# Kernel optimization log

Measured on AMD Instinct MI355X. Metric: run time of the kernel, lower is better.

## Reference

```python
import jax, jax.numpy as jnp
import numpy as np

# static graph structure: B graphs, each with NPER nodes and DEG*NPER edges
B = 128        # graphs in batch
NPER = 400     # nodes per graph (fMRI atlas ROIs)
DEG = 16       # avg degree
EPG = NPER * DEG
E = B * EPG    # 819200 edges total
F_IN = 400     # num_features
H = 128        # hidden dim of GraphConv
C = 2          # num_classes
K1, K2, K3 = 320, 256, 205  # ceil(0.8*400), ceil(0.8*320), ceil(0.8*256)


def setup_inputs() -> dict:
    key = jax.random.key(0)
    ks = jax.random.split(key, 24)
    x = jax.random.normal(ks[0], (B * NPER, F_IN), dtype=jnp.float32)
    # edges constrained within each graph (PyG batched disjoint-union convention)
    src_l = jax.random.randint(ks[1], (B, EPG), 0, NPER)
    dst_l = jax.random.randint(ks[2], (B, EPG), 0, NPER)
    off = (jnp.arange(B, dtype=jnp.int32) * NPER)[:, None]
    edge_src = (src_l + off).reshape(-1).astype(jnp.int32)
    edge_dst = (dst_l + off).reshape(-1).astype(jnp.int32)
    batch = jnp.repeat(jnp.arange(B, dtype=jnp.int32), NPER)
    s = 0.05
    p = {
        'Wrel1': jax.random.normal(ks[3], (H, F_IN)) * s,
        'Wroot1': jax.random.normal(ks[4], (H, F_IN)) * s,
        'b1': jnp.zeros((H,), jnp.float32),
        'pw1': jax.random.normal(ks[5], (H,)) * s,
        'Wrel2': jax.random.normal(ks[6], (H, H)) * s,
        'Wroot2': jax.random.normal(ks[7], (H, H)) * s,
        'b2': jnp.zeros((H,), jnp.float32),
        'pw2': jax.random.normal(ks[8], (H,)) * s,
        'Wrel3': jax.random.normal(ks[9], (H, H)) * s,
        'Wroot3': jax.random.normal(ks[10], (H, H)) * s,
        'b3': jnp.zeros((H,), jnp.float32),
        'pw3': jax.random.normal(ks[11], (H,)) * s,
        'W1': jax.random.normal(ks[12], (128, 256)) * s,
        'bl1': jnp.zeros((128,), jnp.float32),
        'W2': jax.random.normal(ks[13], (64, 128)) * s,
        'bl2': jnp.zeros((64,), jnp.float32),
        'W3': jax.random.normal(ks[14], (C, 64)) * s,
        'bl3': jnp.zeros((C,), jnp.float32),
    }
    return dict(x=x, edge_src=edge_src, edge_dst=edge_dst, batch=batch, **p)


def _graph_conv(x, src, dst, emask, Wrel, b, Wroot):
    # PyG GraphConv: lin_rel(sum_j x_j) + lin_root(x_i); masked edges contribute 0
    msg = x[src] * emask[:, None]
    agg = jax.ops.segment_sum(msg, dst, num_segments=x.shape[0])
    return agg @ Wrel.T + b + x @ Wroot.T


def _topk_pool(x, src, dst, emask, w, npg, k):
    # score = x.w / ||w||; keep top-k per graph; gate kept x by tanh(score)
    score = (x @ w) / (jnp.linalg.norm(w) + 1e-16)
    vals, idx = jax.lax.top_k(score.reshape(B, npg), k)      # [B,k]
    perm = (jnp.arange(B, dtype=jnp.int32)[:, None] * npg + idx).reshape(-1)
    xk = x[perm] * jnp.tanh(vals).reshape(-1)[:, None]
    new_id = jnp.full((B * npg,), -1, jnp.int32).at[perm].set(
        jnp.arange(B * k, dtype=jnp.int32))
    ns, nd = new_id[src], new_id[dst]
    keep = (ns >= 0) & (nd >= 0)
    em2 = emask * keep.astype(emask.dtype)
    return xk, jnp.where(keep, ns, 0), jnp.where(keep, nd, 0), em2


def _readout(x, k):
    xr = x.reshape(B, k, H)
    return jnp.concatenate([xr.max(axis=1), xr.mean(axis=1)], axis=1)  # [B,256]


def reference(x, edge_src, edge_dst, batch,
              Wrel1, Wroot1, b1, pw1, Wrel2, Wroot2, b2, pw2,
              Wrel3, Wroot3, b3, pw3, W1, bl1, W2, bl2, W3, bl3):
    em = jnp.ones((E,), jnp.float32)
    h = jax.nn.relu(_graph_conv(x, edge_src, edge_dst, em, Wrel1, b1, Wroot1))
    h, s, d, em = _topk_pool(h, edge_src, edge_dst, em, pw1, NPER, K1)
    x1 = _readout(h, K1)
    h = jax.nn.relu(_graph_conv(h, s, d, em, Wrel2, b2, Wroot2))
    h, s, d, em = _topk_pool(h, s, d, em, pw2, K1, K2)
    x2 = _readout(h, K2)
    h = jax.nn.relu(_graph_conv(h, s, d, em, Wrel3, b3, Wroot3))
    h, s, d, em = _topk_pool(h, s, d, em, pw3, K2, K3)
    x3 = _readout(h, K3)
    z = x1 + x2 + x3
    z = jax.nn.relu(z @ W1.T + bl1)  # dropout is identity in eval mode
    z = jax.nn.relu(z @ W2.T + bl2)
    return jax.nn.log_softmax(z @ W3.T + bl3, axis=-1)
```

## Files before the change

kernel.cpp:

```cpp
#include <hip/hip_runtime.h>
#include <math.h>

#define BATCH 128
#define NPER 400
#define EPG 6400
#define NEDGE 819200
#define F_IN 400
#define HD 128
#define K1 320
#define K2 256
#define K3 205

typedef __bf16 bf16x8 __attribute__((ext_vector_type(8)));
typedef float f32x4 __attribute__((ext_vector_type(4)));

__device__ __forceinline__ unsigned short f2bf(float f) {
    unsigned u = __builtin_bit_cast(unsigned, f);
    unsigned r = u + 0x7fffu + ((u >> 16) & 1u);
    return (unsigned short)(r >> 16);
}
__device__ __forceinline__ float bf2f(unsigned short s) {
    unsigned u = ((unsigned)s) << 16;
    return __builtin_bit_cast(float, u);
}

__device__ __forceinline__ void async_ld16(const void* g, void* lds) {
    __builtin_amdgcn_global_load_lds(
        (const __attribute__((address_space(1))) unsigned int*)g,
        (__attribute__((address_space(3))) unsigned int*)lds, 16, 0, 0);
}

static constexpr size_t SZ_TREL = 51200ull * 128 * 4;
static constexpr size_t OFF_TREL = 0;
static constexpr size_t OFF_H    = OFF_TREL + SZ_TREL;
static constexpr size_t OFF_HP   = OFF_H + SZ_TREL;
static constexpr size_t OFF_SC   = OFF_HP + 40960ull * 128 * 4;
static constexpr size_t OFF_ES   = OFF_SC + 51200ull * 4;
static constexpr size_t OFF_ED   = OFF_ES + (size_t)NEDGE * 4;
static constexpr size_t OFF_EM   = OFF_ED + (size_t)NEDGE * 4;
static constexpr size_t OFF_Z    = OFF_EM + (size_t)NEDGE * 4;
static constexpr size_t OFF_COFF = OFF_Z + 128ull * 256 * 4;
static constexpr size_t OFF_CDEG = OFF_COFF + 51200ull * 4;
static constexpr size_t OFF_CSRC = OFF_CDEG + 51200ull * 4;
static constexpr size_t OFF_W1H  = OFF_CSRC + (size_t)NEDGE * 4;
static constexpr size_t OFF_W1L  = OFF_W1H + 16ull * 13 * 512 * 2;
static constexpr size_t OFF_W2H  = OFF_W1L + 16ull * 13 * 512 * 2;
static constexpr size_t OFF_W2L  = OFF_W2H + 16ull * 4 * 512 * 2;
static constexpr size_t OFF_W3H  = OFF_W2L + 16ull * 4 * 512 * 2;
static constexpr size_t OFF_W3L  = OFF_W3H + 16ull * 4 * 512 * 2;

__global__ __launch_bounds__(64) void prep_w_all(
    const float* __restrict__ Wrel1, const float* __restrict__ Wroot1,
    const float* __restrict__ Wrel2, const float* __restrict__ Wroot2,
    const float* __restrict__ Wrel3, const float* __restrict__ Wroot3,
    unsigned short* __restrict__ b1h, unsigned short* __restrict__ b1l,
    unsigned short* __restrict__ b2h, unsigned short* __restrict__ b2l,
    unsigned short* __restrict__ b3h, unsigned short* __restrict__ b3l) {
    const int layer = blockIdx.z;
    const int s = blockIdx.x;
    const int ntile = blockIdx.y;
    const int Ks = (layer == 0) ? 13 : 4;
    const int Kd = (layer == 0) ? F_IN : HD;
    if (s >= Ks) return;
    const float* Wrel  = (layer == 0) ? Wrel1  : (layer == 1) ? Wrel2  : Wrel3;
    const float* Wroot = (layer == 0) ? Wroot1 : (layer == 1) ? Wroot2 : Wroot3;
    unsigned short* bh = (layer == 0) ? b1h : (layer == 1) ? b2h : b3h;
    unsigned short* bl = (layer == 0) ? b1l : (layer == 1) ? b2l : b3l;
    const int t = threadIdx.x;
    const int rowin = t & 15, qd = t >> 4;
    const int n = ntile * 16 + rowin;
    const int k = s * 32 + qd * 8;
    const float* src = (n < 128) ? &Wrel[(n & 127) * Kd] : &Wroot[(n & 127) * Kd];
    unsigned short hv[8], lv[8];
#pragma unroll
    for (int e = 0; e < 8; e++) {
        float f = (k + e < Kd) ? src[k + e] : 0.f;
        unsigned short hi = f2bf(f);
        hv[e] = hi;
        lv[e] = f2bf(f - bf2f(hi));
    }
    size_t o = ((size_t)ntile * Ks + s) * 512 + (size_t)t * 8;
#pragma unroll
    for (int e = 0; e < 8; e++) { bh[o + e] = hv[e]; bl[o + e] = lv[e]; }
}

template <int Ks, int Kd>
__global__ __launch_bounds__(256) void gemm_mfma(
    const float* __restrict__ A,
    const unsigned short* __restrict__ bh_p, const unsigned short* __restrict__ bl_p,
    float* __restrict__ t_rel, float* __restrict__ h) {
    __shared__ float Alds[2][2048];
    const int tid = threadIdx.x;
    const int lane = tid & 63;
    const int wv = tid >> 6;
    const int lm = lane & 15;
    const int qd = (lane >> 4) & 3;
    const int m0 = blockIdx.x * 64;
    const int nt0 = wv * 4;

    const int srow = wv * 8 + (lane >> 3);
    const int sgr  = (lane & 7) ^ (lane >> 3);
    const size_t amax = (size_t)gridDim.x * 64 * Kd * 4 - 16;
    const char* Abyte = (const char*)A;

    const int ga = (((2 * qd)     ^ (lm & 7)) << 4);
    const int gb = (((2 * qd + 1) ^ (lm & 7)) << 4);

    f32x4 acc[4][4];
#pragma unroll
    for (int i = 0; i < 4; i++)
#pragma unroll
        for (int j = 0; j < 4; j++) acc[i][j] = (f32x4){0.f, 0.f, 0.f, 0.f};

    auto stage = [&](int buf, int s) {
#pragma unroll
        for (int p = 0; p < 2; ++p) {
            const int row = srow + p * 32;
            size_t go = (size_t)(m0 + row) * Kd * 4 + (size_t)s * 128
                        + ((size_t)sgr << 4);
            if (go > amax) go = amax;
            async_ld16(Abyte + go, &Alds[buf][p * 1024 + wv * 256]);
        }
    };

    stage(0, 0);
    __syncthreads();

#pragma unroll
    for (int s = 0; s < Ks; ++s) {
        if (s + 1 < Ks) stage((s + 1) & 1, s + 1);

        const char* Ab = (const char*)&Alds[s & 1][0];
        bf16x8 ah[4], al[4];
#pragma unroll
        for (int i = 0; i < 4; i++) {
            float4 f0, f1;
            if (s * 32 + qd * 8 < Kd) {
                const char* base = Ab + (lm + i * 16) * 128;
                f0 = *(const float4*)(base + ga);
                f1 = *(const float4*)(base + gb);
            } else {
                f0 = make_float4(0.f, 0.f, 0.f, 0.f);
                f1 = f0;
            }
            float fe[8] = {f0.x, f0.y, f0.z, f0.w, f1.x, f1.y, f1.z, f1.w};
#pragma unroll
            for (int e = 0; e < 8; e++) {
                __bf16 hb = (__bf16)fe[e];
                ah[i][e] = hb;
                al[i][e] = (__bf16)(fe[e] - (float)hb);
            }
        }
        bf16x8 bh[4], bl[4];
#pragma unroll
        for (int j = 0; j < 4; j++)
            bh[j] = *(const bf16x8*)&bh_p[((size_t)(nt0 + j) * Ks + s) * 512 + lane * 8];
#pragma unroll
        for (int j = 0; j < 4; j++)
            bl[j] = *(const bf16x8*)&bl_p[((size_t)(nt0 + j) * Ks + s) * 512 + lane * 8];
#pragma unroll
        for (int j = 0; j < 4; j++)
#pragma unroll
            for (int i = 0; i < 4; i++)
                acc[i][j] = __builtin_amdgcn_mfma_f32_16x16x32_bf16(
                    ah[i], bh[j], acc[i][j], 0, 0, 0);
#pragma unroll
        for (int j = 0; j < 4; j++)
#pragma unroll
            for (int i = 0; i < 4; i++)
                acc[i][j] = __builtin_amdgcn_mfma_f32_16x16x32_bf16(
                    al[i], bh[j], acc[i][j], 0, 0, 0);
#pragma unroll
        for (int j = 0; j < 4; j++)
#pragma unroll
            for (int i = 0; i < 4; i++)
                acc[i][j] = __builtin_amdgcn_mfma_f32_16x16x32_bf16(
                    ah[i], bl[j], acc[i][j], 0, 0, 0);

        __syncthreads();
    }
    float* out = (wv < 2) ? t_rel : h;
    const int colbase = (wv & 1) * 64;
#pragma unroll
    for (int i = 0; i < 4; i++)
#pragma unroll
        for (int j = 0; j < 4; j++) {
            int row = m0 + i * 16 + qd * 4;
            int col = colbase + j * 16 + lm;
#pragma unroll
            for (int r = 0; r < 4; r++)
                out[(size_t)(row + r) * 128 + col] = acc[i][j][r];
        }
}

__global__ __launch_bounds__(1024) void csr_build0(
    const int* __restrict__ gsrc, const int* __restrict__ gdst,
    int* __restrict__ csr_off, int* __restrict__ csr_deg, int* __restrict__ csr_src) {
    __shared__ int cnt[NPER];
    __shared__ int cur[NPER];
    __shared__ int sscan[512];
    const int g = blockIdx.x;
    const int t = threadIdx.x;
    for (int i = t; i < NPER; i += 1024) cnt[i] = 0;
    __syncthreads();
    for (int e = t; e < EPG; e += 1024) {
        int dl = gdst[g * EPG + e] - g * NPER;
        atomicAdd(&cnt[dl], 1);
    }
    __syncthreads();
    if (t < 512) sscan[t] = (t < NPER) ? cnt[t] : 0;
    __syncthreads();
    for (int d = 1; d < 512; d <<= 1) {
        int v = 0;
        if (t < 512 && t >= d) v = sscan[t - d];
        __syncthreads();
        if (t < 512 && t >= d) sscan[t] += v;
        __syncthreads();
    }
    if (t < NPER) {
        int excl = (t == 0) ? 0 : sscan[t - 1];
        int st = g * EPG + excl;
        csr_off[g * NPER + t] = st;
        csr_deg[g * NPER + t] = cnt[t];
        cur[t] = st;
    }
    __syncthreads();
    for (int e = t; e < EPG; e += 1024) {
        int eg = g * EPG + e;
        int dl = gdst[eg] - g * NPER;
        int slot = atomicAdd(&cur[dl], 1);
        csr_src[slot] = gsrc[eg];
    }
}

__global__ __launch_bounds__(256) void agg_score(
    const float* __restrict__ t_rel,
    const int* __restrict__ csr_off, const int* __restrict__ csr_deg,
    const int* __restrict__ csr_src,
    const float* __restrict__ bias, const float* __restrict__ pw,
    float* __restrict__ h, float* __restrict__ sc, int npg) {
    const int xcd = blockIdx.x & 7;
    const int j = blockIdx.x >> 3;
    const int bpg = npg >> 2;
    const int graph = xcd * (BATCH / 8) + j / bpg;
    const int nblk = j - (j / bpg) * bpg;
    const int wid = graph * npg + nblk * 4 + (threadIdx.x >> 6);
    const int lane = threadIdx.x & 63;

    const int start = csr_off[wid];
    const int deg = csr_deg[wid];
    const size_t fo = (size_t)lane * 2;
    float a0 = 0.f, a1 = 0.f, b0 = 0.f, b1 = 0.f;
    float c0 = 0.f, c1 = 0.f, d0 = 0.f, d1 = 0.f;
    int e = 0;
    for (; e + 4 <= deg; e += 4) {
        int s0 = csr_src[start + e];
        int s1 = csr_src[start + e + 1];
        int s2 = csr_src[start + e + 2];
        int s3 = csr_src[start + e + 3];
        float2 v0 = *(const float2*)&t_rel[(size_t)s0 * 128 + fo];
        float2 v1 = *(const float2*)&t_rel[(size_t)s1 * 128 + fo];
        float2 v2 = *(const float2*)&t_rel[(size_t)s2 * 128 + fo];
        float2 v3 = *(const float2*)&t_rel[(size_t)s3 * 128 + fo];
        a0 += v0.x; a1 += v0.y;
        b0 += v1.x; b1 += v1.y;
        c0 += v2.x; c1 += v2.y;
        d0 += v3.x; d1 += v3.y;
    }
    for (; e < deg; e++) {
        int s0 = csr_src[start + e];
        float2 v0 = *(const float2*)&t_rel[(size_t)s0 * 128 + fo];
        a0 += v0.x; a1 += v0.y;
    }
    a0 += b0 + c0 + d0;
    a1 += b1 + c1 + d1;

    float2 bb = *(const float2*)&bias[fo];
    size_t o = (size_t)wid * 128 + fo;
    float2 hv = *(const float2*)&h[o];
    hv.x = fmaxf(hv.x + a0 + bb.x, 0.f);
    hv.y = fmaxf(hv.y + a1 + bb.y, 0.f);
    *(float2*)&h[o] = hv;
    float2 pp = *(const float2*)&pw[fo];
    float d = hv.x * pp.x + hv.y * pp.y;
    float nr = pp.x * pp.x + pp.y * pp.y;
#pragma unroll
    for (int off = 32; off; off >>= 1) {
        d += __shfl_down(d, off, 64);
        nr += __shfl_down(nr, off, 64);
    }
    if (lane == 0) sc[wid] = d / (sqrtf(nr) + 1e-16f);
}

__device__ __forceinline__ bool rank_before(float as, int ai, float bs, int bi) {
    return (as > bs) || (as == bs && ai < bi);
}
__global__ __launch_bounds__(1024) void topk_pool(
    const float* __restrict__ sc, const float* __restrict__ h,
    float* __restrict__ hp, float* __restrict__ z,
    const int* __restrict__ gsrc, const int* __restrict__ gdst,
    int* __restrict__ es, int* __restrict__ ed, int* __restrict__ em,
    int* __restrict__ csr_off, int* __restrict__ csr_deg, int* __restrict__ csr_src,
    int npg, int k, int mode) {
    __shared__ float sk[512];
    __shared__ int si[512];
    __shared__ int nid[NPER];
    __shared__ float tgs[K1];
    __shared__ int packed[EPG];
    __shared__ int cnt[K1];
    __shared__ int cur[K1];
    __shared__ int sscan[512];
    __shared__ float pmx[8][128], psm[8][128];
    const int g = blockIdx.x;
    const int t = threadIdx.x;

    if (t < 512) {
        sk[t] = (t < npg) ? sc[g * npg + t] : -INFINITY;
        si[t] = t;
    }
    __syncthreads();
    for (int size = 2; size <= 512; size <<= 1) {
        for (int stride = size >> 1; stride; stride >>= 1) {
            if (t < 512) {
                int i = t, j = i ^ stride;
                if (j > i) {
                    bool up = ((i & size) == 0);
                    float a = sk[i], b = sk[j];
                    int ai = si[i], bi = si[j];
                    bool doswap = up ? rank_before(b, bi, a, ai)
                                     : rank_before(a, ai, b, bi);
                    if (doswap) { sk[i] = b; sk[j] = a; si[i] = bi; si[j] = ai; }
                }
            }
            __syncthreads();
        }
    }
    if (t < 512) {
        int orig = si[t];
        if (orig < npg) nid[orig] = (t < k) ? t : -1;
        if (t < k) tgs[t] = tanhf(sk[t]);
    }
    if (t < K1) cnt[t] = 0;
    __syncthreads();

    {
        const int f = t & 127;
        const int jq = t >> 7;
        float mx = -INFINITY, sm = 0.f;
        for (int j = jq; j < k; j += 8) {
            float v = h[(size_t)(g * npg + si[j]) * 128 + f] * tgs[j];
            if (mode != 2) hp[(size_t)(g * k + j) * 128 + f] = v;
            mx = fmaxf(mx, v);
            sm += v;
        }
        pmx[jq][f] = mx; psm[jq][f] = sm;
        __syncthreads();
        if (t < 128) {
            mx = pmx[0][t]; sm = psm[0][t];
#pragma unroll
            for (int q = 1; q < 8; q++) {
                mx = fmaxf(mx, pmx[q][t]);
                sm += psm[q][t];
            }
            z[g * 256 + t] += mx;
            z[g * 256 + 128 + t] += sm / (float)k;
        }
    }
    if (mode == 2) return;

    for (int e = t; e < EPG; e += 1024) {
        int eg = g * EPG + e;
        int sl, dl, m;
        if (mode == 0) { sl = gsrc[eg] - g * NPER; dl = gdst[eg] - g * NPER; m = 1; }
        else           { sl = es[eg]; dl = ed[eg]; m = em[eg]; }
        int ns = nid[sl], nd = nid[dl];
        int keep = (m && ns >= 0 && nd >= 0) ? 1 : 0;
        es[eg] = keep ? ns : 0;
        ed[eg] = keep ? nd : 0;
        em[eg] = keep;
        packed[e] = keep ? (ns | (nd << 16)) : -1;
        if (keep) atomicAdd(&cnt[nd], 1);
    }
    __syncthreads();
    if (t < 512) sscan[t] = (t < k) ? cnt[t] : 0;
    __syncthreads();
    for (int d = 1; d < 512; d <<= 1) {
        int v = 0;
        if (t < 512 && t >= d) v = sscan[t - d];
        __syncthreads();
        if (t < 512 && t >= d) sscan[t] += v;
        __syncthreads();
    }
    if (t < k) {
        int excl = (t == 0) ? 0 : sscan[t - 1];
        int st = g * EPG + excl;
        csr_off[g * k + t] = st;
        csr_deg[g * k + t] = cnt[t];
        cur[t] = st;
    }
    __syncthreads();
    for (int e = t; e < EPG; e += 1024) {
        int p = packed[e];
        if (p >= 0) {
            int ns = p & 0xffff, nd = p >> 16;
            int slot = atomicAdd(&cur[nd], 1);
            csr_src[slot] = g * k + ns;
        }
    }
}

__global__ __launch_bounds__(256) void mlp_head(const float* __restrict__ z,
                                                const float* __restrict__ W1,
                                                const float* __restrict__ bl1,
                                                const float* __restrict__ W2,
                                                const float* __restrict__ bl2,
                                                const float* __restrict__ W3,
                                                const float* __restrict__ bl3,
                                                float* __restrict__ out) {
    __shared__ float zs[256], l1[128], l2[64];
    const int g = blockIdx.x, t = threadIdx.x;
    zs[t] = z[g * 256 + t];
    __syncthreads();
    if (t < 128) {
        float s = bl1[t];
        const float* w = &W1[t * 256];
        for (int i = 0; i < 256; i++) s += w[i] * zs[i];
        l1[t] = fmaxf(s, 0.f);
    }
    __syncthreads();
    if (t < 64) {
        float s = bl2[t];
        const float* w = &W2[t * 128];
        for (int i = 0; i < 128; i++) s += w[i] * l1[i];
        l2[t] = fmaxf(s, 0.f);
    }
    __syncthreads();
    if (t == 0) {
        float a = bl3[0], b = bl3[1];
        for (int i = 0; i < 64; i++) { a += W3[i] * l2[i]; b += W3[64 + i] * l2[i]; }
        float m = fmaxf(a, b);
        float lse = m + logf(expf(a - m) + expf(b - m));
        out[g * 2 + 0] = a - lse;
        out[g * 2 + 1] = b - lse;
    }
}

extern "C" void kernel_launch(void* const* d_in, const int* in_sizes, int n_in,
                              void* d_out, int out_size, void* d_ws, size_t ws_size,
                              hipStream_t stream) {
    const float* x        = (const float*)d_in[0];
    const int*   edge_src = (const int*)d_in[1];
    const int*   edge_dst = (const int*)d_in[2];
    const float* Wrel1 = (const float*)d_in[4];
    const float* Wroot1= (const float*)d_in[5];
    const float* b1    = (const float*)d_in[6];
    const float* pw1   = (const float*)d_in[7];
    const float* Wrel2 = (const float*)d_in[8];
    const float* Wroot2= (const float*)d_in[9];
    const float* b2    = (const float*)d_in[10];
    const float* pw2   = (const float*)d_in[11];
    const float* Wrel3 = (const float*)d_in[12];
    const float* Wroot3= (const float*)d_in[13];
    const float* b3    = (const float*)d_in[14];
    const float* pw3   = (const float*)d_in[15];
    const float* W1    = (const float*)d_in[16];
    const float* bl1   = (const float*)d_in[17];
    const float* W2    = (const float*)d_in[18];
    const float* bl2   = (const float*)d_in[19];
    const float* W3    = (const float*)d_in[20];
    const float* bl3   = (const float*)d_in[21];

    char* ws = (char*)d_ws;
    float* t_rel = (float*)(ws + OFF_TREL);
    float* h     = (float*)(ws + OFF_H);
    float* hp    = (float*)(ws + OFF_HP);
    float* sc    = (float*)(ws + OFF_SC);
    int*   es    = (int*)(ws + OFF_ES);
    int*   ed    = (int*)(ws + OFF_ED);
    int*   em    = (int*)(ws + OFF_EM);
    float* z     = (float*)(ws + OFF_Z);
    int*   coff  = (int*)(ws + OFF_COFF);
    int*   cdeg  = (int*)(ws + OFF_CDEG);
    int*   csrc  = (int*)(ws + OFF_CSRC);
    unsigned short* w1h = (unsigned short*)(ws + OFF_W1H);
    unsigned short* w1l = (unsigned short*)(ws + OFF_W1L);
    unsigned short* w2h = (unsigned short*)(ws + OFF_W2H);
    unsigned short* w2l = (unsigned short*)(ws + OFF_W2L);
    unsigned short* w3h = (unsigned short*)(ws + OFF_W3H);
    unsigned short* w3l = (unsigned short*)(ws + OFF_W3L);

    hipMemsetAsync(z, 0, 128ull * 256 * 4, stream);
    prep_w_all<<<dim3(13, 16, 3), 64, 0, stream>>>(
        Wrel1, Wroot1, Wrel2, Wroot2, Wrel3, Wroot3,
        w1h, w1l, w2h, w2l, w3h, w3l);
    csr_build0<<<BATCH, 1024, 0, stream>>>(edge_src, edge_dst, coff, cdeg, csrc);

    gemm_mfma<13, F_IN><<<800, 256, 0, stream>>>(x, w1h, w1l, t_rel, h);
    agg_score<<<51200 / 4, 256, 0, stream>>>(t_rel, coff, cdeg, csrc, b1, pw1,
                                             h, sc, NPER);
    topk_pool<<<BATCH, 1024, 0, stream>>>(sc, h, hp, z, edge_src, edge_dst,
                                          es, ed, em, coff, cdeg, csrc,
                                          NPER, K1, 0);

    gemm_mfma<4, HD><<<640, 256, 0, stream>>>(hp, w2h, w2l, t_rel, h);
    agg_score<<<40960 / 4, 256, 0, stream>>>(t_rel, coff, cdeg, csrc, b2, pw2,
                                             h, sc, K1);
    topk_pool<<<BATCH, 1024, 0, stream>>>(sc, h, hp, z, nullptr, nullptr,
                                          es, ed, em, coff, cdeg, csrc,
                                          K1, K2, 1);

    gemm_mfma<4, HD><<<512, 256, 0, stream>>>(hp, w3h, w3l, t_rel, h);
    agg_score<<<32768 / 4, 256, 0, stream>>>(t_rel, coff, cdeg, csrc, b3, pw3,
                                             h, sc, K2);
    topk_pool<<<BATCH, 1024, 0, stream>>>(sc, h, nullptr, z, nullptr, nullptr,
                                          es, ed, em, coff, cdeg, csrc,
                                          K2, K3, 2);

    mlp_head<<<BATCH, 256, 0, stream>>>(z, W1, bl1, W2, bl2, W3, bl3, (float*)d_out);
}
```

Baseline: 464.4 us.

## Triple-buffer A staging and register-prefetch B fragments in the MFMA GEMM

The GEMM's LDS staging of A moves from double to triple buffering, with loads issued two stages ahead. The per-iteration __syncthreads is replaced by an explicit vmcnt wait plus s_barrier. The bf16 hi/lo B fragments for the next k-step are prefetched into registers while the current step's MFMAs run. MFMA issue is wrapped in s_setprio to favour the math. The goal is to hide global-load latency behind compute, at the cost of extra LDS, more VGPRs and hand-counted waitcnt values that depend on instruction ordering.

```diff
diff --git a/kernel.cpp b/kernel.cpp
--- a/kernel.cpp
+++ b/kernel.cpp
@@ -89,7 +89,7 @@
     const float* __restrict__ A,
     const unsigned short* __restrict__ bh_p, const unsigned short* __restrict__ bl_p,
     float* __restrict__ t_rel, float* __restrict__ h) {
-    __shared__ float Alds[2][2048];
+    __shared__ float Alds[3][2048];
     const int tid = threadIdx.x;
     const int lane = tid & 63;
     const int wv = tid >> 6;
@@ -99,7 +99,7 @@
     const int nt0 = wv * 4;
 
     const int srow = wv * 8 + (lane >> 3);
-    const int sgr  = (lane & 7) ^ (lane >> 3);
+    const int sgr  = (lane & 7) ^ ((lane >> 3) & 7);
     const size_t amax = (size_t)gridDim.x * 64 * Kd * 4 - 16;
     const char* Abyte = (const char*)A;
 
@@ -124,13 +124,33 @@
     };
 
     stage(0, 0);
-    __syncthreads();
+    bf16x8 bh_c[4], bl_c[4];
+#pragma unroll
+    for (int j = 0; j < 4; j++)
+        bh_c[j] = *(const bf16x8*)&bh_p[((size_t)(nt0 + j) * Ks + 0) * 512 + lane * 8];
+#pragma unroll
+    for (int j = 0; j < 4; j++)
+        bl_c[j] = *(const bf16x8*)&bl_p[((size_t)(nt0 + j) * Ks + 0) * 512 + lane * 8];
+    if (Ks > 1) stage(1, 1);
 
 #pragma unroll
     for (int s = 0; s < Ks; ++s) {
-        if (s + 1 < Ks) stage((s + 1) & 1, s + 1);
-
-        const char* Ab = (const char*)&Alds[s & 1][0];
+        if (s + 1 < Ks) asm volatile("s_waitcnt vmcnt(2)" ::: "memory");
+        else            asm volatile("s_waitcnt vmcnt(0)" ::: "memory");
+        __builtin_amdgcn_s_barrier();
+
+        bf16x8 bh_n[4], bl_n[4];
+        if (s + 1 < Ks) {
+#pragma unroll
+            for (int j = 0; j < 4; j++)
+                bh_n[j] = *(const bf16x8*)&bh_p[((size_t)(nt0 + j) * Ks + (s + 1)) * 512 + lane * 8];
+#pragma unroll
+            for (int j = 0; j < 4; j++)
+                bl_n[j] = *(const bf16x8*)&bl_p[((size_t)(nt0 + j) * Ks + (s + 1)) * 512 + lane * 8];
+        }
+        if (s + 2 < Ks) stage((s + 2) % 3, s + 2);
+
+        const char* Ab = (const char*)&Alds[s % 3][0];
         bf16x8 ah[4], al[4];
 #pragma unroll
         for (int i = 0; i < 4; i++) {
@@ -151,33 +171,31 @@
                 al[i][e] = (__bf16)(fe[e] - (float)hb);
             }
         }
-        bf16x8 bh[4], bl[4];
-#pragma unroll
-        for (int j = 0; j < 4; j++)
-            bh[j] = *(const bf16x8*)&bh_p[((size_t)(nt0 + j) * Ks + s) * 512 + lane * 8];
-#pragma unroll
-        for (int j = 0; j < 4; j++)
-            bl[j] = *(const bf16x8*)&bl_p[((size_t)(nt0 + j) * Ks + s) * 512 + lane * 8];
+        __builtin_amdgcn_s_setprio(1);
 #pragma unroll
         for (int j = 0; j < 4; j++)
 #pragma unroll
             for (int i = 0; i < 4; i++)
                 acc[i][j] = __builtin_amdgcn_mfma_f32_16x16x32_bf16(
-                    ah[i], bh[j], acc[i][j], 0, 0, 0);
+                    ah[i], bh_c[j], acc[i][j], 0, 0, 0);
 #pragma unroll
         for (int j = 0; j < 4; j++)
 #pragma unroll
             for (int i = 0; i < 4; i++)
                 acc[i][j] = __builtin_amdgcn_mfma_f32_16x16x32_bf16(
-                    al[i], bh[j], acc[i][j], 0, 0, 0);
+                    al[i], bh_c[j], acc[i][j], 0, 0, 0);
 #pragma unroll
         for (int j = 0; j < 4; j++)
 #pragma unroll
             for (int i = 0; i < 4; i++)
                 acc[i][j] = __builtin_amdgcn_mfma_f32_16x16x32_bf16(
-                    ah[i], bl[j], acc[i][j], 0, 0, 0);
-
-        __syncthreads();
+                    ah[i], bl_c[j], acc[i][j], 0, 0, 0);
+        __builtin_amdgcn_s_setprio(0);
+
+        if (s + 1 < Ks) {
+#pragma unroll
+            for (int j = 0; j < 4; j++) { bh_c[j] = bh_n[j]; bl_c[j] = bl_n[j]; }
+        }
     }
     float* out = (wv < 2) ? t_rel : h;
     const int colbase = (wv & 1) * 64;
```

Measured after the change: 446.7 us. 1.04x faster.

## Make GEMM A-staging per-wave with vmcnt waits instead of block barriers

Applied to the files above, without the earlier changes.

The split-bf16 MFMA GEMM now gives each wave a private LDS copy of the A tile. Waves wait on their own async loads with explicit s_waitcnt vmcnt and no longer call __syncthreads. The M tile per block is halved to 32 rows, doubling the grid, and B fragments are loaded ahead of the staging. MFMA sections run at raised priority via s_setprio. This removes block-level barrier stalls and improves occupancy, at the cost of each wave reloading the same A rows, which quadruples A global and LDS traffic per block. The hand-counted vmcnt values must match the compiler's load ordering exactly.

```diff
diff --git a/kernel.cpp b/kernel.cpp
--- a/kernel.cpp
+++ b/kernel.cpp
@@ -85,65 +85,73 @@
 }
 
 template <int Ks, int Kd>
-__global__ __launch_bounds__(256) void gemm_mfma(
+__global__ __launch_bounds__(256, 4) void gemm_wave(
     const float* __restrict__ A,
     const unsigned short* __restrict__ bh_p, const unsigned short* __restrict__ bl_p,
     float* __restrict__ t_rel, float* __restrict__ h) {
-    __shared__ float Alds[2][2048];
+    __shared__ float Alds[4][2][1024];
     const int tid = threadIdx.x;
     const int lane = tid & 63;
     const int wv = tid >> 6;
     const int lm = lane & 15;
     const int qd = (lane >> 4) & 3;
-    const int m0 = blockIdx.x * 64;
+    const int m0 = blockIdx.x * 32;
     const int nt0 = wv * 4;
 
-    const int srow = wv * 8 + (lane >> 3);
-    const int sgr  = (lane & 7) ^ (lane >> 3);
-    const size_t amax = (size_t)gridDim.x * 64 * Kd * 4 - 16;
+    const int srow = lane >> 3;
+    const int sgr  = (lane & 7) ^ srow;
+    const size_t amax = (size_t)gridDim.x * 32 * Kd * 4 - 16;
     const char* Abyte = (const char*)A;
 
     const int ga = (((2 * qd)     ^ (lm & 7)) << 4);
     const int gb = (((2 * qd + 1) ^ (lm & 7)) << 4);
 
-    f32x4 acc[4][4];
-#pragma unroll
-    for (int i = 0; i < 4; i++)
+    f32x4 acc[2][4];
+#pragma unroll
+    for (int i = 0; i < 2; i++)
 #pragma unroll
         for (int j = 0; j < 4; j++) acc[i][j] = (f32x4){0.f, 0.f, 0.f, 0.f};
 
     auto stage = [&](int buf, int s) {
 #pragma unroll
-        for (int p = 0; p < 2; ++p) {
-            const int row = srow + p * 32;
-            size_t go = (size_t)(m0 + row) * Kd * 4 + (size_t)s * 128
+        for (int q = 0; q < 4; ++q) {
+            size_t go = (size_t)(m0 + q * 8 + srow) * Kd * 4 + (size_t)s * 128
                         + ((size_t)sgr << 4);
             if (go > amax) go = amax;
-            async_ld16(Abyte + go, &Alds[buf][p * 1024 + wv * 256]);
+            async_ld16(Abyte + go, &Alds[wv][buf][q * 256]);
         }
     };
 
     stage(0, 0);
-    __syncthreads();
 
 #pragma unroll
     for (int s = 0; s < Ks; ++s) {
+        bf16x8 bhc[4], blc[4];
+#pragma unroll
+        for (int j = 0; j < 4; j++)
+            bhc[j] = *(const bf16x8*)&bh_p[((size_t)(nt0 + j) * Ks + s) * 512 + lane * 8];
+#pragma unroll
+        for (int j = 0; j < 4; j++)
+            blc[j] = *(const bf16x8*)&bl_p[((size_t)(nt0 + j) * Ks + s) * 512 + lane * 8];
         if (s + 1 < Ks) stage((s + 1) & 1, s + 1);
 
-        const char* Ab = (const char*)&Alds[s & 1][0];
-        bf16x8 ah[4], al[4];
-#pragma unroll
-        for (int i = 0; i < 4; i++) {
-            float4 f0, f1;
+        if (s + 1 < Ks) asm volatile("s_waitcnt vmcnt(12)" ::: "memory");
+        else            asm volatile("s_waitcnt vmcnt(8)" ::: "memory");
+
+        const char* Ab = (const char*)&Alds[wv][s & 1][0];
+        bf16x8 ah[2], al[2];
+#pragma unroll
+        for (int i = 0; i < 2; i++) {
+            f32x4 f0, f1;
             if (s * 32 + qd * 8 < Kd) {
                 const char* base = Ab + (lm + i * 16) * 128;
-                f0 = *(const float4*)(base + ga);
-                f1 = *(const float4*)(base + gb);
+                f0 = *(const f32x4*)(base + ga);
+                f1 = *(const f32x4*)(base + gb);
             } else {
-                f0 = make_float4(0.f, 0.f, 0.f, 0.f);
+                f0 = (f32x4){0.f, 0.f, 0.f, 0.f};
                 f1 = f0;
             }
-            float fe[8] = {f0.x, f0.y, f0.z, f0.w, f1.x, f1.y, f1.z, f1.w};
+            float fe[8] = {f0[0], f0[1], f0[2], f0[3], f1[0], f1[1], f1[2], f1[3]};
 #pragma unroll
             for (int e = 0; e < 8; e++) {
                 __bf16 hb = (__bf16)fe[e];
@@ -151,38 +159,31 @@
                 al[i][e] = (__bf16)(fe[e] - (float)hb);
             }
         }
-        bf16x8 bh[4], bl[4];
+        __builtin_amdgcn_s_setprio(1);
 #pragma unroll
         for (int j = 0; j < 4; j++)
-            bh[j] = *(const bf16x8*)&bh_p[((size_t)(nt0 + j) * Ks + s) * 512 + lane * 8];
+#pragma unroll
+            for (int i = 0; i < 2; i++)
+                acc[i][j] = __builtin_amdgcn_mfma_f32_16x16x32_bf16(
+                    ah[i], bhc[j], acc[i][j], 0, 0, 0);
 #pragma unroll
         for (int j = 0; j < 4; j++)
-            bl[j] = *(const bf16x8*)&bl_p[((size_t)(nt0 + j) * Ks + s) * 512 + lane * 8];
+#pragma unroll
+            for (int i = 0; i < 2; i++)
+                acc[i][j] = __builtin_amdgcn_mfma_f32_16x16x32_bf16(
+                    al[i], bhc[j], acc[i][j], 0, 0, 0);
 #pragma unroll
         for (int j = 0; j < 4; j++)
 #pragma unroll
-            for (int i = 0; i < 4; i++)
+            for (int i = 0; i < 2; i++)
                 acc[i][j] = __builtin_amdgcn_mfma_f32_16x16x32_bf16(
-                    ah[i], bh[j], acc[i][j], 0, 0, 0);
-#pragma unroll
-        for (int j = 0; j < 4; j++)
-#pragma unroll
-            for (int i = 0; i < 4; i++)
-                acc[i][j] = __builtin_amdgcn_mfma_f32_16x16x32_bf16(
-                    al[i], bh[j], acc[i][j], 0, 0, 0);
-#pragma unroll
-        for (int j = 0; j < 4; j++)
-#pragma unroll
-            for (int i = 0; i < 4; i++)
-                acc[i][j] = __builtin_amdgcn_mfma_f32_16x16x32_bf16(
-                    ah[i], bl[j], acc[i][j], 0, 0, 0);
-
-        __syncthreads();
+                    ah[i], blc[j], acc[i][j], 0, 0, 0);
+        __builtin_amdgcn_s_setprio(0);
     }
     float* out = (wv < 2) ? t_rel : h;
     const int colbase = (wv & 1) * 64;
 #pragma unroll
-    for (int i = 0; i < 4; i++)
+    for (int i = 0; i < 2; i++)
 #pragma unroll
         for (int j = 0; j < 4; j++) {
             int row = m0 + i * 16 + qd * 4;
@@ -495,21 +496,21 @@
         w1h, w1l, w2h, w2l, w3h, w3l);
     csr_build0<<<BATCH, 1024, 0, stream>>>(edge_src, edge_dst, coff, cdeg, csrc);
 
-    gemm_mfma<13, F_IN><<<800, 256, 0, stream>>>(x, w1h, w1l, t_rel, h);
+    gemm_wave<13, F_IN><<<1600, 256, 0, stream>>>(x, w1h, w1l, t_rel, h);
     agg_score<<<51200 / 4, 256, 0, stream>>>(t_rel, coff, cdeg, csrc, b1, pw1,
                                              h, sc, NPER);
     topk_pool<<<BATCH, 1024, 0, stream>>>(sc, h, hp, z, edge_src, edge_dst,
                                           es, ed, em, coff, cdeg, csrc,
                                           NPER, K1, 0);
 
-    gemm_mfma<4, HD><<<640, 256, 0, stream>>>(hp, w2h, w2l, t_rel, h);
+    gemm_wave<4, HD><<<1280, 256, 0, stream>>>(hp, w2h, w2l, t_rel, h);
     agg_score<<<40960 / 4, 256, 0, stream>>>(t_rel, coff, cdeg, csrc, b2, pw2,
                                              h, sc, K1);
     topk_pool<<<BATCH, 1024, 0, stream>>>(sc, h, hp, z, nullptr, nullptr,
                                           es, ed, em, coff, cdeg, csrc,
                                           K1, K2, 1);
 
-    gemm_mfma<4, HD><<<512, 256, 0, stream>>>(hp, w3h, w3l, t_rel, h);
+    gemm_wave<4, HD><<<1024, 256, 0, stream>>>(hp, w3h, w3l, t_rel, h);
     agg_score<<<32768 / 4, 256, 0, stream>>>(t_rel, coff, cdeg, csrc, b3, pw3,
                                              h, sc, K2);
     topk_pool<<<BATCH, 1024, 0, stream>>>(sc, h, nullptr, z, nullptr, nullptr,
```

New measurement: 488.6 us. +5.2%, slower.
